# Optimization experiments

Hardware: AMD Instinct MI355X
Metric: run time of the kernel (lower is better)

The kernel has to match this reference:

```python
import jax, jax.numpy as jnp
import numpy as np

N, F, H, R, T, E, C = 50000, 128, 64, 3, 2, 500000, 2


def _seg_sum(v, idx, n):
    return jax.ops.segment_sum(v, idx, num_segments=n)


def _sage(x, src, dst, Wl, Wr, b, n):
    # PyG SAGEConv(mean): lin_l(mean_{j->i} x_j) + lin_r(x_i); lin_l carries bias.
    s = _seg_sum(x[src], dst, n)
    cnt = _seg_sum(jnp.ones((src.shape[0],), x.dtype), dst, n)
    agg = s / jnp.maximum(cnt, 1.0)[:, None]
    return agg @ Wl + x @ Wr + b


def _gcn(x, src, dst, w, W, b, n):
    # PyG GCNConv with edge_weight: self-loops (weight 1) + symmetric norm.
    deg = _seg_sum(w, dst, n) + 1.0
    dinv = deg ** -0.5
    norm = dinv[src] * w * dinv[dst]
    xW = x @ W
    return _seg_sum(norm[:, None] * xW[src], dst, n) + xW / deg[:, None] + b


def setup_inputs() -> dict:
    key = jax.random.key(0)
    ks = jax.random.split(key, 32)
    rn = lambda k, shp, s=0.1: jax.random.normal(k, shp, dtype=jnp.float32) * s
    return {
        "x": rn(ks[0], (N, F), 1.0),
        "edge_main": jax.random.randint(ks[1], (R, 2, E), 0, N, dtype=jnp.int32),
        "edge_tree": jax.random.randint(ks[2], (R, T, 2, E), 0, N, dtype=jnp.int32),
        "sage_Wl0": rn(ks[3], (R, F, H)), "sage_Wr0": rn(ks[4], (R, F, H)), "sage_b0": rn(ks[5], (R, H)),
        "sage_Wl1": rn(ks[6], (R, H, H)), "sage_Wr1": rn(ks[7], (R, H, H)), "sage_b1": rn(ks[8], (R, H)),
        "tree_Wl": rn(ks[9], (R, T, F, H)), "tree_Wr": rn(ks[10], (R, T, F, H)), "tree_b": rn(ks[11], (R, T, H)),
        "gate_W": rn(ks[12], (R, T, H)), "gate_b": rn(ks[13], (R, T)),
        "node_emb": rn(ks[14], (R, H), 1.0), "edge_emb": rn(ks[15], (R, H), 1.0),
        "fm_W": rn(ks[16], (R, 2 * H + F, F)), "fm_b": rn(ks[17], (R, F)),
        "ea_W1": rn(ks[18], (3 * H, F)), "ea_b1": rn(ks[19], (F,)),
        "ea_W2": rn(ks[20], (F, 1)), "ea_b2": rn(ks[21], (1,)),
        "gcn_W0": rn(ks[22], (R, F, H)), "gcn_b0": rn(ks[23], (R, H)),
        "gcn_W1": rn(ks[24], (R, H, H)), "gcn_b1": rn(ks[25], (R, H)),
        "lin_W": rn(ks[26], (R * H, C)), "lin_b": rn(ks[27], (C,)),
    }


def reference(x, edge_main, edge_tree, sage_Wl0, sage_Wr0, sage_b0, sage_Wl1, sage_Wr1, sage_b1,
              tree_Wl, tree_Wr, tree_b, gate_W, gate_b, node_emb, edge_emb, fm_W, fm_b,
              ea_W1, ea_b1, ea_W2, ea_b2, gcn_W0, gcn_b0, gcn_W1, gcn_b1, lin_W, lin_b):
    outs = []
    for r in range(R):
        src, dst = edge_main[r, 0], edge_main[r, 1]
        # Layer_AGG main SAGE stack (2 layers, relu between; dropout = eval no-op)
        y = jax.nn.relu(_sage(x, src, dst, sage_Wl0[r], sage_Wr0[r], sage_b0[r], N))
        y = _sage(y, src, dst, sage_Wl1[r], sage_Wr1[r], sage_b1[r], N)
        # tree branches + softmax gating
        trees = []
        for t in range(T):
            ts, td = edge_tree[r, t, 0], edge_tree[r, t, 1]
            trees.append(jax.nn.relu(_sage(x, ts, td, tree_Wl[r, t], tree_Wr[r, t], tree_b[r, t], N)))
        gates = jnp.stack([trees[t] @ gate_W[r, t] + gate_b[r, t] for t in range(T)], axis=-1)  # [N,T]
        alpha = jax.nn.softmax(gates, axis=-1)
        x_tree = sum(trees[t] * alpha[:, t:t + 1] for t in range(T))
        lo = y + 1.0 * x_tree  # self.weight = 1
        # edge mask via edge_attr_mlp on [lo[src], lo[dst], edge_type_emb]
        ef = jnp.concatenate([lo[src], lo[dst], jnp.broadcast_to(edge_emb[r], (E, H))], axis=-1)
        em = jax.nn.relu(ef @ ea_W1 + ea_b1) @ ea_W2 + ea_b2  # [E,1]
        # feature mask via feat_mask_r on [lo, x, node_type_emb]
        hetro = jnp.concatenate([lo, x, jnp.broadcast_to(node_emb[r], (N, H))], axis=-1)
        fm = hetro @ fm_W[r] + fm_b[r]
        mx = x * fm
        w = ((em - em.min()) / (em.max() - em.min()))[:, 0]  # min-max norm -> [E]
        # hetero GCN stack with edge weights
        z = jax.nn.relu(_gcn(mx, src, dst, w, gcn_W0[r], gcn_b0[r], N))
        z = _gcn(z, src, dst, w, gcn_W1[r], gcn_b1[r], N)
        outs.append(z)
    x_temp = jnp.concatenate(outs, axis=1)  # [N, R*H]
    logits = jnp.clip(x_temp @ lin_W + lin_b, -1e10, 1e10)
    return jax.nn.log_softmax(logits, axis=1), x_temp
```

## Files before the change

kernel.cpp:

```cpp
#include <hip/hip_runtime.h>
#include <cstdint>

#define N_NODES 50000
#define FEAT    128
#define HID     64
#define NREL    3
#define NTREE   2
#define NEDGE   500000
#define NCLS    2

#define BKT   391
#define CAP   1600
#define CHUNK 8192

typedef __attribute__((ext_vector_type(8))) short bfrag;
typedef __attribute__((ext_vector_type(4))) float ffrag;

__device__ __forceinline__ float wave_red(float v){
  #pragma unroll
  for(int off = 32; off > 0; off >>= 1) v += __shfl_xor(v, off, 64);
  return v;
}

__device__ __forceinline__ unsigned short f2b(float f){
  unsigned int u = __float_as_uint(f);
  unsigned int r = (u + 0x7FFFu + ((u >> 16) & 1u)) >> 16;
  return (unsigned short)r;
}
__device__ __forceinline__ float b2f_lo(unsigned int u){ return __uint_as_float(u << 16); }
__device__ __forceinline__ float b2f_hi(unsigned int u){ return __uint_as_float(u & 0xFFFF0000u); }
__device__ __forceinline__ float b2f(unsigned short s){ return __uint_as_float(((unsigned int)s) << 16); }

struct EdgePtrs { const int* s[9]; const int* d[9]; };

__global__ __launch_bounds__(256)
void k_passA(EdgePtrs ep, int* __restrict__ cursor, int* __restrict__ bucketed){
  int set = blockIdx.y;
  const int* src = ep.s[set];
  const int* dst = ep.d[set];
  __shared__ int stage[CHUNK];
  __shared__ int hist[BKT], gbase[BKT], lbase[BKT], cur[BKT];
  int tid = threadIdx.x;
  for(int b = tid; b < BKT; b += 256) hist[b] = 0;
  __syncthreads();
  int e0 = blockIdx.x * CHUNK;
  int nE = NEDGE - e0; if(nE > CHUNK) nE = CHUNK;
  for(int i = tid; i < nE; i += 256) atomicAdd(&hist[dst[e0 + i] >> 7], 1);
  __syncthreads();
  for(int b = tid; b < BKT; b += 256){
    int c = hist[b];
    gbase[b] = c ? atomicAdd(&cursor[set * BKT + b], c) : 0;
  }
  if(tid < 64){
    int running = 0;
    for(int base = 0; base < BKT; base += 64){
      int idx = base + tid;
      int v = (idx < BKT) ? hist[idx] : 0;
      int orig = v;
      #pragma unroll
      for(int off = 1; off < 64; off <<= 1){
        int t = __shfl_up(v, off, 64);
        if(tid >= off) v += t;
      }
      if(idx < BKT){ lbase[idx] = running + v - orig; cur[idx] = running + v - orig; }
      running += __shfl(v, 63, 64);
    }
  }
  __syncthreads();
  for(int i = tid; i < nE; i += 256){
    int e = e0 + i;
    int d = dst[e];
    int r = atomicAdd(&cur[d >> 7], 1);
    stage[r] = (d << 16) | src[e];
  }
  __syncthreads();
  int* bk = bucketed + (size_t)set * BKT * CAP;
  for(int i = tid; i < nE; i += 256){
    int p = stage[i];
    int b = ((unsigned int)p) >> 23;
    int pos = gbase[b] + (i - lbase[b]);
    if(pos < CAP) bk[b * CAP + pos] = p;
  }
}

__global__ void k_scanB(const int* __restrict__ cursor, int* __restrict__ bktbase,
                        int* __restrict__ indptr9){
  int set = blockIdx.x;
  __shared__ int sm[512];
  int tid = threadIdx.x;
  int v = (tid < BKT) ? cursor[set * BKT + tid] : 0;
  sm[tid] = v; __syncthreads();
  for(int off = 1; off < 512; off <<= 1){
    int t = (tid >= off) ? sm[tid - off] : 0;
    __syncthreads();
    sm[tid] += t;
    __syncthreads();
  }
  if(tid < BKT) bktbase[set * BKT + tid] = sm[tid] - v;
  if(tid == 0) indptr9[(size_t)set * (N_NODES + 1) + N_NODES] = NEDGE;
}

__global__ __launch_bounds__(256)
void k_passB(const int* __restrict__ bucketed, const int* __restrict__ cursor,
             const int* __restrict__ bktbase, int* __restrict__ indptr9,
             int* __restrict__ csr9){
  int set = blockIdx.y, b = blockIdx.x;
  int cnt = cursor[set * BKT + b]; if(cnt > CAP) cnt = CAP;
  int ebase = bktbase[set * BKT + b];
  const int* bk = bucketed + (size_t)set * BKT * CAP + b * CAP;
  __shared__ int pk[CAP];
  __shared__ int stage[CAP];
  __shared__ int h[128], sc[128], cur[128];
  int tid = threadIdx.x;
  for(int i = tid; i < cnt; i += 256) pk[i] = bk[i];
  if(tid < 128) h[tid] = 0;
  __syncthreads();
  for(int i = tid; i < cnt; i += 256) atomicAdd(&h[(pk[i] >> 16) & 127], 1);
  __syncthreads();
  if(tid < 128) sc[tid] = h[tid];
  __syncthreads();
  for(int off = 1; off < 128; off <<= 1){
    int t = 0;
    if(tid < 128 && tid >= off) t = sc[tid - off];
    __syncthreads();
    if(tid < 128) sc[tid] += t;
    __syncthreads();
  }
  if(tid < 128){
    int excl = sc[tid] - h[tid];
    cur[tid] = excl;
    int node = b * 128 + tid;
    if(node < N_NODES) indptr9[(size_t)set * (N_NODES + 1) + node] = ebase + excl;
  }
  __syncthreads();
  for(int i = tid; i < cnt; i += 256){
    int p = pk[i];
    int r = atomicAdd(&cur[(p >> 16) & 127], 1);
    stage[r] = p & 0xFFFF;
  }
  __syncthreads();
  int* out = csr9 + (size_t)set * NEDGE + ebase;
  for(int i = tid; i < cnt; i += 256) out[i] = stage[i];
}

__global__ void k_tobf16(const float* __restrict__ in, unsigned short* __restrict__ o, int n4){
  int i = blockIdx.x * 256 + threadIdx.x;
  if(i < n4){
    float4 v = ((const float4*)in)[i];
    ushort4 u; u.x = f2b(v.x); u.y = f2b(v.y); u.z = f2b(v.z); u.w = f2b(v.w);
    ((ushort4*)o)[i] = u;
  }
}

struct PackJobs { const float* src[20]; int wst[20]; int K[20]; int dst[20]; int n; };

__global__ void k_wpack(PackJobs J, unsigned short* __restrict__ out){
  int j = blockIdx.x;
  if(j >= J.n) return;
  const float* s = J.src[j];
  int wst = J.wst[j], K = J.K[j];
  unsigned short* o = out + J.dst[j];
  for(int i = threadIdx.x; i < K * 64; i += 256){
    int k = i >> 6, c = i & 63;
    o[((((k >> 3) * 64) + c) << 3) + (k & 7)] = f2b(s[(size_t)k * wst + c]);
  }
}

struct MG {
  const unsigned short* Wt[4];
  const float* bias[4];
  const void* add[4];
  const float* mul[4];
  void* out[4];
  int ast, mst, ost;
};

template<int K1, int K2, int NGRP, int RELU, int HAS_ADD, int ADDB, int HAS_MUL, int OUT_BF16>
__global__ __launch_bounds__(256)
void k_mgemm(const unsigned short* __restrict__ X1, int xs1,
             const unsigned short* __restrict__ X2, int xs2, MG P){
  constexpr int K = K1 + K2;
  constexpr int KS = K / 32;
  int tid = threadIdx.x;
  int lane = tid & 63;
  int w = tid >> 6;
  int row0 = blockIdx.x * 64 + w * 16;
  int l15 = lane & 15, kg = lane >> 4;
  int arow = row0 + l15; if(arow > N_NODES - 1) arow = N_NODES - 1;
  bfrag a[KS];
  #pragma unroll
  for(int ks = 0; ks < KS; ks++){
    int kk = ks * 32 + kg * 8;
    const unsigned short* p = (kk < K1) ? (X1 + (size_t)arow * xs1 + kk)
                                        : (X2 + (size_t)arow * xs2 + (kk - K1));
    a[ks] = *(const bfrag*)p;
  }
  int orow0 = row0 + kg * 4;
  #pragma unroll
  for(int g = 0; g < NGRP; g++){
    const unsigned short* Wg = P.Wt[g];
    #pragma unroll
    for(int ct = 0; ct < 4; ct++){
      int col = ct * 16 + l15;
      ffrag acc = {0.f, 0.f, 0.f, 0.f};
      #pragma unroll
      for(int ks = 0; ks < KS; ks++){
        bfrag bf = *(const bfrag*)(Wg + (((size_t)(ks * 4 + kg) * 64 + col) << 3));
        acc = __builtin_amdgcn_mfma_f32_16x16x32_bf16(a[ks], bf, acc, 0, 0, 0);
      }
      float bv = P.bias[g] ? P.bias[g][col] : 0.f;
      #pragma unroll
      for(int i = 0; i < 4; i++){
        int r = orow0 + i;
        if(r >= N_NODES) break;
        float v = acc[i] + bv;
        if(HAS_ADD){
          if(ADDB) v += b2f(((const unsigned short*)P.add[g])[(size_t)r * P.ast + col]);
          else     v += ((const float*)P.add[g])[(size_t)r * P.ast + col];
        }
        if(RELU) v = fmaxf(v, 0.f);
        if(HAS_MUL) v *= P.mul[g][(size_t)r * P.mst + col];
        if(OUT_BF16) ((unsigned short*)P.out[g])[(size_t)r * P.ost + col] = f2b(v);
        else         ((float*)P.out[g])[(size_t)r * P.ost + col] = v;
      }
    }
  }
}

template<int OUTB>
__global__ void k_aggq(const unsigned short* __restrict__ TB, int tst,
                       const int* __restrict__ indptr, const int* __restrict__ csr,
                       void* __restrict__ out){
  int br = blockIdx.y;
  const unsigned short* T = TB + (size_t)br * tst;
  const int* ip = indptr + (size_t)br * (N_NODES + 1);
  const int* cs = csr + (size_t)br * NEDGE;
  int lane = threadIdx.x & 63, wid = threadIdx.x >> 6;
  int node = blockIdx.x * 4 + wid;
  if(node >= N_NODES) return;
  int q = lane >> 4, c = lane & 15;
  int beg = ip[node], end = ip[node + 1];
  int cnt = end - beg;
  float sc = 1.0f / (float)(cnt >= 1 ? cnt : 1);
  float a0 = 0.f, a1 = 0.f, a2 = 0.f, a3 = 0.f;
  for(int j = beg + q; j < end; j += 4){
    int s = cs[j];
    uint2 u = *(const uint2*)(T + (size_t)s * 64 + c * 4);
    a0 += b2f_lo(u.x); a1 += b2f_hi(u.x);
    a2 += b2f_lo(u.y); a3 += b2f_hi(u.y);
  }
  a0 += __shfl_xor(a0, 16, 64); a1 += __shfl_xor(a1, 16, 64);
  a2 += __shfl_xor(a2, 16, 64); a3 += __shfl_xor(a3, 16, 64);
  a0 += __shfl_xor(a0, 32, 64); a1 += __shfl_xor(a1, 32, 64);
  a2 += __shfl_xor(a2, 32, 64); a3 += __shfl_xor(a3, 32, 64);
  if(q == 0){
    if(OUTB){
      ushort4 o; o.x = f2b(a0 * sc); o.y = f2b(a1 * sc); o.z = f2b(a2 * sc); o.w = f2b(a3 * sc);
      *(ushort4*)((unsigned short*)out + (size_t)br * tst + (size_t)node * 64 + c * 4) = o;
    } else {
      *(float4*)((float*)out + (size_t)node * 64 + c * 4) = float4{a0 * sc, a1 * sc, a2 * sc, a3 * sc};
    }
  }
}

__global__ void k_gates_lo(const unsigned short* __restrict__ t0b, const unsigned short* __restrict__ t1b,
                           const float* __restrict__ y, const float* __restrict__ gate_W,
                           const float* __restrict__ gate_b, unsigned short* __restrict__ lo){
  int lane = threadIdx.x & 63, wid = threadIdx.x >> 6;
  int node = blockIdx.x * 4 + wid;
  if(node >= N_NODES) return;
  size_t idx = (size_t)node * 64 + lane;
  float t0v = b2f(t0b[idx]), t1v = b2f(t1b[idx]), yv = y[idx];
  float g0 = wave_red(t0v * gate_W[lane]) + gate_b[0];
  float g1 = wave_red(t1v * gate_W[64 + lane]) + gate_b[1];
  float m = fmaxf(g0, g1);
  float e0 = expf(g0 - m), e1 = expf(g1 - m);
  float a0 = e0 / (e0 + e1);
  lo[idx] = f2b(yv + a0 * t0v + (1.f - a0) * t1v);
}

__global__ void k_cvec2(const float* __restrict__ ee, const float* __restrict__ ne,
                        const float* __restrict__ eaW1, const float* __restrict__ eab1,
                        const float* __restrict__ fmW, const float* __restrict__ fmb,
                        float* __restrict__ cE, float* __restrict__ cF){
  int j = threadIdx.x;
  if(blockIdx.x == 0){
    float s = eab1[j];
    for(int k = 0; k < 64; k++) s += ee[k] * eaW1[(128 + k) * 128 + j];
    cE[j] = s;
  } else {
    float s = fmb[j];
    for(int k = 0; k < 64; k++) s += ne[k] * fmW[(192 + k) * 128 + j];
    cF[j] = s;
  }
}

__global__ void k_em2(const unsigned short* __restrict__ AB,
                      const int* __restrict__ indptr, const int* __restrict__ csr_src,
                      const float* __restrict__ cvec, const float* __restrict__ W2,
                      const float* __restrict__ b2, float* __restrict__ em,
                      float* __restrict__ sumem){
  int lane = threadIdx.x & 63, wid = threadIdx.x >> 6;
  int node = blockIdx.x * 4 + wid;
  if(node >= N_NODES) return;
  int h = lane >> 5, c = lane & 31;
  uint2 bu = *(const uint2*)(AB + (size_t)node * 256 + 128 + c * 4);
  float4 cv = *(const float4*)&cvec[c * 4];
  float4 wv = *(const float4*)&W2[c * 4];
  float c0 = b2f_lo(bu.x) + cv.x, c1 = b2f_hi(bu.x) + cv.y;
  float c2 = b2f_lo(bu.y) + cv.z, c3 = b2f_hi(bu.y) + cv.w;
  float b2v = b2[0];
  int beg = indptr[node], end = indptr[node + 1];
  float ssum = 0.f;
  for(int j = beg + h; j < end; j += 2){
    int s = csr_src[j];
    uint2 au = *(const uint2*)(AB + (size_t)s * 256 + c * 4);
    float v = fmaxf(b2f_lo(au.x) + c0, 0.f) * wv.x + fmaxf(b2f_hi(au.x) + c1, 0.f) * wv.y
            + fmaxf(b2f_lo(au.y) + c2, 0.f) * wv.z + fmaxf(b2f_hi(au.y) + c3, 0.f) * wv.w;
    #pragma unroll
    for(int off = 1; off < 32; off <<= 1) v += __shfl_xor(v, off, 64);
    if(c == 0){
      float r = v + b2v;
      em[j] = r;
      ssum += r;
    }
  }
  float so = __shfl_xor(ssum, 32, 64);
  if(lane == 0) sumem[node] = ssum + so;
}

__global__ void k_minmax_part(const float* __restrict__ em, int n,
                              float* __restrict__ pmn, float* __restrict__ pmx){
  __shared__ float smn[256], smx[256];
  int tid = threadIdx.x;
  float mn = 3.4e38f, mx = -3.4e38f;
  for(int i = blockIdx.x * 256 + tid; i < n; i += gridDim.x * 256){
    float v = em[i];
    mn = fminf(mn, v); mx = fmaxf(mx, v);
  }
  smn[tid] = mn; smx[tid] = mx; __syncthreads();
  for(int s = 128; s > 0; s >>= 1){
    if(tid < s){ smn[tid] = fminf(smn[tid], smn[tid + s]); smx[tid] = fmaxf(smx[tid], smx[tid + s]); }
    __syncthreads();
  }
  if(tid == 0){ pmn[blockIdx.x] = smn[0]; pmx[blockIdx.x] = smx[0]; }
}

__global__ void k_minmax_final(const float* __restrict__ pmn, const float* __restrict__ pmx,
                               int nb, float* __restrict__ scal){
  __shared__ float smn[256], smx[256];
  int tid = threadIdx.x;
  float mn = 3.4e38f, mx = -3.4e38f;
  if(tid < nb){ mn = pmn[tid]; mx = pmx[tid]; }
  smn[tid] = mn; smx[tid] = mx; __syncthreads();
  for(int s = 128; s > 0; s >>= 1){
    if(tid < s){ smn[tid] = fminf(smn[tid], smn[tid + s]); smx[tid] = fmaxf(smx[tid], smx[tid + s]); }
    __syncthreads();
  }
  if(tid == 0){
    scal[0] = smn[0];
    scal[1] = 1.0f / fmaxf(smx[0] - smn[0], 1e-30f);
  }
}

__global__ void k_dinv(const int* __restrict__ indptr, const float* __restrict__ sumem,
                       const float* __restrict__ scal, float* __restrict__ dinv){
  int i = blockIdx.x * 256 + threadIdx.x;
  if(i >= N_NODES) return;
  float mn = scal[0], inv = scal[1];
  float cnt = (float)(indptr[i + 1] - indptr[i]);
  dinv[i] = rsqrtf(1.f + (sumem[i] - cnt * mn) * inv);
}

template<int RELU, int OUTB>
__global__ void k_gcn(const unsigned short* __restrict__ xW, const int* __restrict__ indptr,
                      const int* __restrict__ csr_src, const float* __restrict__ em,
                      const float* __restrict__ scal, const float* __restrict__ dinv,
                      const float* __restrict__ bias, void* __restrict__ out, int ostride){
  int lane = threadIdx.x & 63, wid = threadIdx.x >> 6;
  int node = blockIdx.x * 4 + wid;
  if(node >= N_NODES) return;
  int q = lane >> 4, c = lane & 15;
  float mn = scal[0], inv = scal[1];
  float di = dinv[node];
  float a0 = 0.f, a1 = 0.f, a2 = 0.f, a3 = 0.f;
  int beg = indptr[node], end = indptr[node + 1];
  for(int j = beg + q; j < end; j += 4){
    int s = csr_src[j];
    float wv = (em[j] - mn) * inv * dinv[s];
    uint2 u = *(const uint2*)(xW + (size_t)s * 64 + c * 4);
    a0 += wv * b2f_lo(u.x); a1 += wv * b2f_hi(u.x);
    a2 += wv * b2f_lo(u.y); a3 += wv * b2f_hi(u.y);
  }
  a0 += __shfl_xor(a0, 16, 64); a1 += __shfl_xor(a1, 16, 64);
  a2 += __shfl_xor(a2, 16, 64); a3 += __shfl_xor(a3, 16, 64);
  a0 += __shfl_xor(a0, 32, 64); a1 += __shfl_xor(a1, 32, 64);
  a2 += __shfl_xor(a2, 32, 64); a3 += __shfl_xor(a3, 32, 64);
  if(q == 0){
    uint2 su = *(const uint2*)(xW + (size_t)node * 64 + c * 4);
    float4 bv = *(const float4*)&bias[c * 4];
    float dd = di * di;
    float r0 = a0 * di + b2f_lo(su.x) * dd + bv.x;
    float r1 = a1 * di + b2f_hi(su.x) * dd + bv.y;
    float r2 = a2 * di + b2f_lo(su.y) * dd + bv.z;
    float r3 = a3 * di + b2f_hi(su.y) * dd + bv.w;
    if(RELU){ r0 = fmaxf(r0, 0.f); r1 = fmaxf(r1, 0.f); r2 = fmaxf(r2, 0.f); r3 = fmaxf(r3, 0.f); }
    if(OUTB){
      ushort4 o; o.x = f2b(r0); o.y = f2b(r1); o.z = f2b(r2); o.w = f2b(r3);
      *(ushort4*)((unsigned short*)out + (size_t)node * ostride + c * 4) = o;
    } else {
      *(float4*)((float*)out + (size_t)node * ostride + c * 4) = float4{r0, r1, r2, r3};
    }
  }
}

__global__ void k_logits(const float* __restrict__ xt, const float* __restrict__ lin_W,
                         const float* __restrict__ lin_b, float* __restrict__ out){
  int lane = threadIdx.x & 63, wid = threadIdx.x >> 6;
  int node = blockIdx.x * 4 + wid;
  if(node >= N_NODES) return;
  float a0 = 0.f, a1 = 0.f;
  #pragma unroll
  for(int q = 0; q < 3; q++){
    int k = q * 64 + lane;
    float v = xt[(size_t)node * 192 + k];
    a0 += v * lin_W[k * 2 + 0];
    a1 += v * lin_W[k * 2 + 1];
  }
  a0 = wave_red(a0);
  a1 = wave_red(a1);
  if(lane == 0){
    float l0 = fminf(fmaxf(a0 + lin_b[0], -1e10f), 1e10f);
    float l1 = fminf(fmaxf(a1 + lin_b[1], -1e10f), 1e10f);
    float m = fmaxf(l0, l1);
    float d = expf(l0 - m) + expf(l1 - m);
    float ls = m + logf(d);
    out[(size_t)node * 2 + 0] = l0 - ls;
    out[(size_t)node * 2 + 1] = l1 - ls;
  }
}

extern "C" void kernel_launch(void* const* d_in, const int* in_sizes, int n_in,
                              void* d_out, int out_size, void* d_ws, size_t ws_size,
                              hipStream_t stream){
  (void)in_sizes; (void)n_in; (void)out_size;
  const int N = N_NODES, E = NEDGE;

  const float* x        = (const float*)d_in[0];
  const int*  edge_main = (const int*)d_in[1];
  const int*  edge_tree = (const int*)d_in[2];
  const float* sage_Wl0 = (const float*)d_in[3];
  const float* sage_Wr0 = (const float*)d_in[4];
  const float* sage_b0  = (const float*)d_in[5];
  const float* sage_Wl1 = (const float*)d_in[6];
  const float* sage_Wr1 = (const float*)d_in[7];
  const float* sage_b1  = (const float*)d_in[8];
  const float* tree_Wl  = (const float*)d_in[9];
  const float* tree_Wr  = (const float*)d_in[10];
  const float* tree_b   = (const float*)d_in[11];
  const float* gate_W   = (const float*)d_in[12];
  const float* gate_b   = (const float*)d_in[13];
  const float* node_emb = (const float*)d_in[14];
  const float* edge_emb = (const float*)d_in[15];
  const float* fm_W     = (const float*)d_in[16];
  const float* fm_b     = (const float*)d_in[17];
  const float* ea_W1    = (const float*)d_in[18];
  const float* ea_b1    = (const float*)d_in[19];
  const float* ea_W2    = (const float*)d_in[20];
  const float* ea_b2    = (const float*)d_in[21];
  const float* gcn_W0   = (const float*)d_in[22];
  const float* gcn_b0   = (const float*)d_in[23];
  const float* gcn_W1   = (const float*)d_in[24];
  const float* gcn_b1   = (const float*)d_in[25];
  const float* lin_W    = (const float*)d_in[26];
  const float* lin_b    = (const float*)d_in[27];

  float* out_lsm   = (float*)d_out;
  float* out_xtemp = (float*)d_out + (size_t)N * NCLS;

  char* ws = (char*)d_ws;
  unsigned short* TB3  = (unsigned short*)(ws + 0);
  unsigned short* TBs  = (unsigned short*)(ws + 0);
  float*          Y    = (float*)(ws + 0);
  unsigned short* xW0b = (unsigned short*)(ws + 0);
  unsigned short* z0b  = (unsigned short*)(ws + 6400000);
  unsigned short* xW1b = (unsigned short*)(ws + 12800000);
  unsigned short* AG3  = (unsigned short*)(ws + 19200000);
  float*          AG   = (float*)(ws + 19200000);
  unsigned short* LOb  = (unsigned short*)(ws + 25600000);
  unsigned short* AB   = (unsigned short*)(ws + 0);
  unsigned short* y0b  = (unsigned short*)(ws + 38400000);
  unsigned short* T0b  = (unsigned short*)(ws + 44800000);
  unsigned short* T1b  = (unsigned short*)(ws + 51200000);
  unsigned short* MXb  = (unsigned short*)(ws + 38400000);
  unsigned short* xb   = (unsigned short*)(ws + 57600000);
  int*   bucketed = (int*)(ws + 0);
  unsigned short* Wpk = (unsigned short*)(ws + 70400000);
  int*   csr9     = (int*)(ws + 71000064);
  int*   indptr9  = (int*)(ws + 89000064);
  float* em       = (float*)(ws + 90800128);
  float* sumem    = (float*)(ws + 92800128);
  float* dinv     = (float*)(ws + 93000128);
  int*   cursor   = (int*)(ws + 93200128);
  int*   bktbase  = (int*)(ws + 93214208);
  float* cvecE    = (float*)(ws + 93228288);
  float* cvecF    = (float*)(ws + 93228800);
  float* scal     = (float*)(ws + 93229312);
  float* pmn      = (float*)(ws + 93229568);
  float* pmx      = (float*)(ws + 93230592);
  if(ws_size < 93231616) return;

  const int GN4 = (N + 3) / 4;
  const int GN  = (N + 255) / 256;
  const int GGM = (N + 63) / 64;
  const int NCH = (E + CHUNK - 1) / CHUNK;

  PackJobs PJ[2]; PJ[0].n = 0; PJ[1].n = 0;
  int npj = 0, dstElem = 0;
  const unsigned short* WlpA[NREL]; const unsigned short* WlpB[NREL]; const unsigned short* WlpC[NREL];
  const unsigned short* Wr0j[NREL]; const unsigned short* WrT0[NREL]; const unsigned short* WrT1[NREL];
  const unsigned short* Wl1j[NREL]; const unsigned short* Wr1j[NREL];
  const unsigned short* Fm0j[NREL]; const unsigned short* Fm1j[NREL];
  const unsigned short* G0j[NREL];  const unsigned short* G1j[NREL];
  const unsigned short *EaA0, *EaA1, *EaB0, *EaB1;
  auto addjob = [&](const float* src, int wst, int K) -> const unsigned short* {
    int slot = npj < 20 ? 0 : 1;
    int k = npj - slot * 20;
    PJ[slot].src[k] = src; PJ[slot].wst[k] = wst; PJ[slot].K[k] = K; PJ[slot].dst[k] = dstElem;
    PJ[slot].n = k + 1;
    const unsigned short* ret = Wpk + dstElem;
    dstElem += K * 64; npj++;
    return ret;
  };
  for(int r = 0; r < NREL; r++){
    WlpA[r] = addjob(sage_Wl0 + (size_t)r * 8192, 64, 128);
    WlpB[r] = addjob(tree_Wl + (size_t)(r * NTREE + 0) * 8192, 64, 128);
    WlpC[r] = addjob(tree_Wl + (size_t)(r * NTREE + 1) * 8192, 64, 128);
    Wr0j[r] = addjob(sage_Wr0 + (size_t)r * 8192, 64, 128);
    WrT0[r] = addjob(tree_Wr + (size_t)(r * NTREE + 0) * 8192, 64, 128);
    WrT1[r] = addjob(tree_Wr + (size_t)(r * NTREE + 1) * 8192, 64, 128);
    Wl1j[r] = addjob(sage_Wl1 + (size_t)r * 4096, 64, 64);
    Wr1j[r] = addjob(sage_Wr1 + (size_t)r * 4096, 64, 64);
    Fm0j[r] = addjob(fm_W + (size_t)r * 32768, 128, 192);
    Fm1j[r] = addjob(fm_W + (size_t)r * 32768 + 64, 128, 192);
    G0j[r]  = addjob(gcn_W0 + (size_t)r * 8192, 64, 128);
    G1j[r]  = addjob(gcn_W1 + (size_t)r * 4096, 64, 64);
  }
  EaA0 = addjob(ea_W1, 128, 64);
  EaA1 = addjob(ea_W1 + 64, 128, 64);
  EaB0 = addjob(ea_W1 + 64 * 128, 128, 64);
  EaB1 = addjob(ea_W1 + 64 * 128 + 64, 128, 64);

  EdgePtrs ep;
  for(int r = 0; r < NREL; r++){
    ep.s[r * 3 + 0] = edge_main + (size_t)r * 2 * E;
    ep.d[r * 3 + 0] = ep.s[r * 3 + 0] + E;
    for(int t = 0; t < NTREE; t++){
      ep.s[r * 3 + 1 + t] = edge_tree + ((size_t)(r * NTREE + t) * 2) * E;
      ep.d[r * 3 + 1 + t] = ep.s[r * 3 + 1 + t] + E;
    }
  }
  hipMemsetAsync(cursor, 0, 9 * BKT * 4, stream);
  k_passA<<<dim3(NCH, 9), 256, 0, stream>>>(ep, cursor, bucketed);
  k_scanB<<<9, 512, 0, stream>>>(cursor, bktbase, indptr9);
  k_passB<<<dim3(BKT, 9), 256, 0, stream>>>(bucketed, cursor, bktbase, indptr9, csr9);

  k_wpack<<<PJ[0].n, 256, 0, stream>>>(PJ[0], Wpk);
  k_wpack<<<PJ[1].n, 256, 0, stream>>>(PJ[1], Wpk);
  k_tobf16<<<(N * 128 / 4 + 255) / 256, 256, 0, stream>>>(x, xb, N * 128 / 4);

  for(int r = 0; r < NREL; r++){
    const int* ipM = indptr9 + (size_t)(r * 3) * (N + 1);
    const int* csM = csr9 + (size_t)(r * 3) * E;

    { MG p{}; p.ost = 64;
      p.Wt[0] = WlpA[r]; p.Wt[1] = WlpB[r]; p.Wt[2] = WlpC[r];
      p.out[0] = TB3; p.out[1] = TB3 + (size_t)N * 64; p.out[2] = TB3 + (size_t)2 * N * 64;
      k_mgemm<128, 0, 3, 0, 0, 0, 0, 1><<<GGM, 256, 0, stream>>>(xb, 128, nullptr, 0, p); }

    k_aggq<1><<<dim3(GN4, 3), 256, 0, stream>>>(TB3, N * 64, ipM, csM, AG3);
    { MG p{}; p.ast = 64; p.ost = 64;
      p.Wt[0] = Wr0j[r]; p.bias[0] = sage_b0 + r * 64; p.add[0] = AG3;                         p.out[0] = y0b;
      p.Wt[1] = WrT0[r]; p.bias[1] = tree_b + (size_t)(r * NTREE + 0) * 64; p.add[1] = AG3 + (size_t)N * 64;   p.out[1] = T0b;
      p.Wt[2] = WrT1[r]; p.bias[2] = tree_b + (size_t)(r * NTREE + 1) * 64; p.add[2] = AG3 + (size_t)2 * N * 64; p.out[2] = T1b;
      k_mgemm<128, 0, 3, 1, 1, 1, 0, 1><<<GGM, 256, 0, stream>>>(xb, 128, nullptr, 0, p); }

    { MG p{}; p.ost = 64; p.Wt[0] = Wl1j[r]; p.out[0] = TBs;
      k_mgemm<64, 0, 1, 0, 0, 0, 0, 1><<<GGM, 256, 0, stream>>>(y0b, 64, nullptr, 0, p); }
    k_aggq<0><<<dim3(GN4, 1), 256, 0, stream>>>(TBs, N * 64, ipM, csM, AG);
    { MG p{}; p.ast = 64; p.ost = 64;
      p.Wt[0] = Wr1j[r]; p.bias[0] = sage_b1 + r * 64; p.add[0] = AG; p.out[0] = Y;
      k_mgemm<64, 0, 1, 0, 1, 0, 0, 0><<<GGM, 256, 0, stream>>>(y0b, 64, nullptr, 0, p); }

    k_gates_lo<<<GN4, 256, 0, stream>>>(T0b, T1b, Y, gate_W + (size_t)r * 128, gate_b + r * 2, LOb);

    k_cvec2<<<2, 128, 0, stream>>>(edge_emb + r * 64, node_emb + r * 64, ea_W1, ea_b1,
                                   fm_W + (size_t)r * 32768, fm_b + r * 128, cvecE, cvecF);

    { MG p{}; p.ost = 256;
      p.Wt[0] = EaA0; p.Wt[1] = EaA1; p.Wt[2] = EaB0; p.Wt[3] = EaB1;
      p.out[0] = AB; p.out[1] = AB + 64; p.out[2] = AB + 128; p.out[3] = AB + 192;
      k_mgemm<64, 0, 4, 0, 0, 0, 0, 1><<<GGM, 256, 0, stream>>>(LOb, 64, nullptr, 0, p); }

    k_em2<<<GN4, 256, 0, stream>>>(AB, ipM, csM, cvecE, ea_W2, ea_b2, em, sumem);

    k_minmax_part<<<256, 256, 0, stream>>>(em, E, pmn, pmx);
    k_minmax_final<<<1, 256, 0, stream>>>(pmn, pmx, 256, scal);

    k_dinv<<<GN, 256, 0, stream>>>(ipM, sumem, scal, dinv);

    { MG p{}; p.mst = 128; p.ost = 128;
      p.Wt[0] = Fm0j[r]; p.Wt[1] = Fm1j[r];
      p.bias[0] = cvecF; p.bias[1] = cvecF + 64;
      p.mul[0] = x; p.mul[1] = x + 64;
      p.out[0] = MXb; p.out[1] = MXb + 64;
      k_mgemm<64, 128, 2, 0, 0, 0, 1, 1><<<GGM, 256, 0, stream>>>(LOb, 64, xb, 128, p); }

    { MG p{}; p.ost = 64; p.Wt[0] = G0j[r]; p.out[0] = xW0b;
      k_mgemm<128, 0, 1, 0, 0, 0, 0, 1><<<GGM, 256, 0, stream>>>(MXb, 128, nullptr, 0, p); }
    k_gcn<1, 1><<<GN4, 256, 0, stream>>>(xW0b, ipM, csM, em, scal, dinv, gcn_b0 + r * 64, z0b, 64);
    { MG p{}; p.ost = 64; p.Wt[0] = G1j[r]; p.out[0] = xW1b;
      k_mgemm<64, 0, 1, 0, 0, 0, 0, 1><<<GGM, 256, 0, stream>>>(z0b, 64, nullptr, 0, p); }
    k_gcn<0, 0><<<GN4, 256, 0, stream>>>(xW1b, ipM, csM, em, scal, dinv, gcn_b1 + r * 64,
                                         out_xtemp + r * 64, 192);
  }

  k_logits<<<GN4, 256, 0, stream>>>(out_xtemp, lin_W, lin_b, out_lsm);
}
```

Baseline: 987.5 us.

## Fuse edge-attr and feature-mask GEMMs, fold minmax into em, unroll gathers

```diff
diff --git a/kernel.cpp b/kernel.cpp
--- a/kernel.cpp
+++ b/kernel.cpp
@@ -11,7 +11,7 @@
 
 #define BKT   391
 #define CAP   1600
-#define CHUNK 8192
+#define CHUNK 4096
 
 typedef __attribute__((ext_vector_type(8))) short bfrag;
 typedef __attribute__((ext_vector_type(4))) float ffrag;
@@ -227,6 +227,71 @@
   }
 }
 
+struct ABMX {
+  const unsigned short* Wea[4];
+  const unsigned short* Wfm[2];
+  const float* cF;
+  const float* xf32;
+  unsigned short* ab;
+  unsigned short* mx;
+};
+
+__global__ __launch_bounds__(256)
+void k_abmx(const unsigned short* __restrict__ LOb, const unsigned short* __restrict__ xb, ABMX P){
+  int tid = threadIdx.x, lane = tid & 63, w = tid >> 6;
+  int row0 = blockIdx.x * 64 + w * 16;
+  int l15 = lane & 15, kg = lane >> 4;
+  int arow = row0 + l15; if(arow > N_NODES - 1) arow = N_NODES - 1;
+  bfrag a[6];
+  a[0] = *(const bfrag*)(LOb + (size_t)arow * 64 + kg * 8);
+  a[1] = *(const bfrag*)(LOb + (size_t)arow * 64 + 32 + kg * 8);
+  #pragma unroll
+  for(int ks = 0; ks < 4; ks++)
+    a[2 + ks] = *(const bfrag*)(xb + (size_t)arow * 128 + ks * 32 + kg * 8);
+  int orow0 = row0 + kg * 4;
+  #pragma unroll
+  for(int g = 0; g < 4; g++){
+    const unsigned short* Wg = P.Wea[g];
+    #pragma unroll
+    for(int ct = 0; ct < 4; ct++){
+      int col = ct * 16 + l15;
+      ffrag acc = {0.f, 0.f, 0.f, 0.f};
+      bfrag b0 = *(const bfrag*)(Wg + (((size_t)(0 * 4 + kg) * 64 + col) << 3));
+      bfrag b1 = *(const bfrag*)(Wg + (((size_t)(1 * 4 + kg) * 64 + col) << 3));
+      acc = __builtin_amdgcn_mfma_f32_16x16x32_bf16(a[0], b0, acc, 0, 0, 0);
+      acc = __builtin_amdgcn_mfma_f32_16x16x32_bf16(a[1], b1, acc, 0, 0, 0);
+      #pragma unroll
+      for(int i = 0; i < 4; i++){
+        int r = orow0 + i;
+        if(r >= N_NODES) break;
+        P.ab[(size_t)r * 256 + g * 64 + col] = f2b(acc[i]);
+      }
+    }
+  }
+  #pragma unroll
+  for(int g = 0; g < 2; g++){
+    const unsigned short* Wg = P.Wfm[g];
+    #pragma unroll
+    for(int ct = 0; ct < 4; ct++){
+      int col = ct * 16 + l15;
+      ffrag acc = {0.f, 0.f, 0.f, 0.f};
+      #pragma unroll
+      for(int ks = 0; ks < 6; ks++){
+        bfrag bf = *(const bfrag*)(Wg + (((size_t)(ks * 4 + kg) * 64 + col) << 3));
+        acc = __builtin_amdgcn_mfma_f32_16x16x32_bf16(a[ks], bf, acc, 0, 0, 0);
+      }
+      float bv = P.cF[g * 64 + col];
+      #pragma unroll
+      for(int i = 0; i < 4; i++){
+        int r = orow0 + i;
+        if(r >= N_NODES) break;
+        float v = (acc[i] + bv) * P.xf32[(size_t)r * 128 + g * 64 + col];
+        P.mx[(size_t)r * 128 + g * 64 + col] = f2b(v);
+      }
+    }
+  }
+}
+
 template<int OUTB>
 __global__ void k_aggq(const unsigned short* __restrict__ TB, int tst,
                        const int* __restrict__ indptr, const int* __restrict__ csr,
@@ -243,7 +308,15 @@
   int cnt = end - beg;
   float sc = 1.0f / (float)(cnt >= 1 ? cnt : 1);
   float a0 = 0.f, a1 = 0.f, a2 = 0.f, a3 = 0.f;
-  for(int j = beg + q; j < end; j += 4){
+  int j = beg + q;
+  for(; j + 4 < end; j += 8){
+    int s0 = cs[j], s1 = cs[j + 4];
+    uint2 u0 = *(const uint2*)(T + (size_t)s0 * 64 + c * 4);
+    uint2 u1 = *(const uint2*)(T + (size_t)s1 * 64 + c * 4);
+    a0 += b2f_lo(u0.x) + b2f_lo(u1.x); a1 += b2f_hi(u0.x) + b2f_hi(u1.x);
+    a2 += b2f_lo(u0.y) + b2f_lo(u1.y); a3 += b2f_hi(u0.y) + b2f_hi(u1.y);
+  }
+  if(j < end){
     int s = cs[j];
     uint2 u = *(const uint2*)(T + (size_t)s * 64 + c * 4);
     a0 += b2f_lo(u.x); a1 += b2f_hi(u.x);
@@ -263,9 +336,29 @@
   }
 }
 
-__global__ void k_gates_lo(const unsigned short* __restrict__ t0b, const unsigned short* __restrict__ t1b,
-                           const float* __restrict__ y, const float* __restrict__ gate_W,
-                           const float* __restrict__ gate_b, unsigned short* __restrict__ lo){
+__global__ void k_gates_cvec(const unsigned short* __restrict__ t0b, const unsigned short* __restrict__ t1b,
+                             const float* __restrict__ y, const float* __restrict__ gate_W,
+                             const float* __restrict__ gate_b, unsigned short* __restrict__ lo,
+                             const float* __restrict__ ee, const float* __restrict__ ne,
+                             const float* __restrict__ eaW1, const float* __restrict__ eab1,
+                             const float* __restrict__ fmW, const float* __restrict__ fmb,
+                             float* __restrict__ cE, float* __restrict__ cF, int gn4){
+  if(blockIdx.x >= gn4){
+    int which = blockIdx.x - gn4;
+    int j = threadIdx.x;
+    if(j < 128){
+      if(which == 0){
+        float s = eab1[j];
+        for(int k = 0; k < 64; k++) s += ee[k] * eaW1[(128 + k) * 128 + j];
+        cE[j] = s;
+      } else {
+        float s = fmb[j];
+        for(int k = 0; k < 64; k++) s += ne[k] * fmW[(192 + k) * 128 + j];
+        cF[j] = s;
+      }
+    }
+    return;
+  }
   int lane = threadIdx.x & 63, wid = threadIdx.x >> 6;
   int node = blockIdx.x * 4 + wid;
   if(node >= N_NODES) return;
@@ -279,71 +372,72 @@
   lo[idx] = f2b(yv + a0 * t0v + (1.f - a0) * t1v);
 }
 
-__global__ void k_cvec2(const float* __restrict__ ee, const float* __restrict__ ne,
-                        const float* __restrict__ eaW1, const float* __restrict__ eab1,
-                        const float* __restrict__ fmW, const float* __restrict__ fmb,
-                        float* __restrict__ cE, float* __restrict__ cF){
-  int j = threadIdx.x;
-  if(blockIdx.x == 0){
-    float s = eab1[j];
-    for(int k = 0; k < 64; k++) s += ee[k] * eaW1[(128 + k) * 128 + j];
-    cE[j] = s;
-  } else {
-    float s = fmb[j];
-    for(int k = 0; k < 64; k++) s += ne[k] * fmW[(192 + k) * 128 + j];
-    cF[j] = s;
-  }
-}
-
 __global__ void k_em2(const unsigned short* __restrict__ AB,
                       const int* __restrict__ indptr, const int* __restrict__ csr_src,
                       const float* __restrict__ cvec, const float* __restrict__ W2,
                       const float* __restrict__ b2, float* __restrict__ em,
-                      float* __restrict__ sumem){
+                      float* __restrict__ sumem, float* __restrict__ pmn, float* __restrict__ pmx){
   int lane = threadIdx.x & 63, wid = threadIdx.x >> 6;
   int node = blockIdx.x * 4 + wid;
-  if(node >= N_NODES) return;
-  int h = lane >> 5, c = lane & 31;
-  uint2 bu = *(const uint2*)(AB + (size_t)node * 256 + 128 + c * 4);
-  float4 cv = *(const float4*)&cvec[c * 4];
-  float4 wv = *(const float4*)&W2[c * 4];
-  float c0 = b2f_lo(bu.x) + cv.x, c1 = b2f_hi(bu.x) + cv.y;
-  float c2 = b2f_lo(bu.y) + cv.z, c3 = b2f_hi(bu.y) + cv.w;
-  float b2v = b2[0];
-  int beg = indptr[node], end = indptr[node + 1];
-  float ssum = 0.f;
-  for(int j = beg + h; j < end; j += 2){
-    int s = csr_src[j];
-    uint2 au = *(const uint2*)(AB + (size_t)s * 256 + c * 4);
-    float v = fmaxf(b2f_lo(au.x) + c0, 0.f) * wv.x + fmaxf(b2f_hi(au.x) + c1, 0.f) * wv.y
-            + fmaxf(b2f_lo(au.y) + c2, 0.f) * wv.z + fmaxf(b2f_hi(au.y) + c3, 0.f) * wv.w;
-    #pragma unroll
-    for(int off = 1; off < 32; off <<= 1) v += __shfl_xor(v, off, 64);
-    if(c == 0){
-      float r = v + b2v;
-      em[j] = r;
-      ssum += r;
-    }
-  }
-  float so = __shfl_xor(ssum, 32, 64);
-  if(lane == 0) sumem[node] = ssum + so;
-}
-
-__global__ void k_minmax_part(const float* __restrict__ em, int n,
-                              float* __restrict__ pmn, float* __restrict__ pmx){
-  __shared__ float smn[256], smx[256];
-  int tid = threadIdx.x;
+  bool act = (node < N_NODES);
   float mn = 3.4e38f, mx = -3.4e38f;
-  for(int i = blockIdx.x * 256 + tid; i < n; i += gridDim.x * 256){
-    float v = em[i];
-    mn = fminf(mn, v); mx = fmaxf(mx, v);
-  }
-  smn[tid] = mn; smx[tid] = mx; __syncthreads();
-  for(int s = 128; s > 0; s >>= 1){
-    if(tid < s){ smn[tid] = fminf(smn[tid], smn[tid + s]); smx[tid] = fmaxf(smx[tid], smx[tid + s]); }
-    __syncthreads();
-  }
-  if(tid == 0){ pmn[blockIdx.x] = smn[0]; pmx[blockIdx.x] = smx[0]; }
+  if(act){
+    int h = lane >> 5, c = lane & 31;
+    uint2 bu = *(const uint2*)(AB + (size_t)node * 256 + 128 + c * 4);
+    float4 cv = *(const float4*)&cvec[c * 4];
+    float4 wv = *(const float4*)&W2[c * 4];
+    float c0 = b2f_lo(bu.x) + cv.x, c1 = b2f_hi(bu.x) + cv.y;
+    float c2 = b2f_lo(bu.y) + cv.z, c3 = b2f_hi(bu.y) + cv.w;
+    float b2v = b2[0];
+    int beg = indptr[node], end = indptr[node + 1];
+    float ssum = 0.f;
+    int j = beg + h;
+    for(; j + 2 < end; j += 4){
+      int s0 = csr_src[j], s1 = csr_src[j + 2];
+      uint2 au0 = *(const uint2*)(AB + (size_t)s0 * 256 + c * 4);
+      uint2 au1 = *(const uint2*)(AB + (size_t)s1 * 256 + c * 4);
+      float v0 = fmaxf(b2f_lo(au0.x) + c0, 0.f) * wv.x + fmaxf(b2f_hi(au0.x) + c1, 0.f) * wv.y
+               + fmaxf(b2f_lo(au0.y) + c2, 0.f) * wv.z + fmaxf(b2f_hi(au0.y) + c3, 0.f) * wv.w;
+      float v1 = fmaxf(b2f_lo(au1.x) + c0, 0.f) * wv.x + fmaxf(b2f_hi(au1.x) + c1, 0.f) * wv.y
+               + fmaxf(b2f_lo(au1.y) + c2, 0.f) * wv.z + fmaxf(b2f_hi(au1.y) + c3, 0.f) * wv.w;
+      #pragma unroll
+      for(int off = 1; off < 32; off <<= 1){
+        v0 += __shfl_xor(v0, off, 64);
+        v1 += __shfl_xor(v1, off, 64);
+      }
+      if(c == 0){
+        float r0 = v0 + b2v, r1 = v1 + b2v;
+        em[j] = r0; em[j + 2] = r1;
+        ssum += r0 + r1;
+        mn = fminf(mn, fminf(r0, r1)); mx = fmaxf(mx, fmaxf(r0, r1));
+      }
+    }
+    if(j < end){
+      int s = csr_src[j];
+      uint2 au = *(const uint2*)(AB + (size_t)s * 256 + c * 4);
+      float v = fmaxf(b2f_lo(au.x) + c0, 0.f) * wv.x + fmaxf(b2f_hi(au.x) + c1, 0.f) * wv.y
+              + fmaxf(b2f_lo(au.y) + c2, 0.f) * wv.z + fmaxf(b2f_hi(au.y) + c3, 0.f) * wv.w;
+      #pragma unroll
+      for(int off = 1; off < 32; off <<= 1) v += __shfl_xor(v, off, 64);
+      if(c == 0){
+        float r = v + b2v;
+        em[j] = r;
+        ssum += r;
+        mn = fminf(mn, r); mx = fmaxf(mx, r);
+      }
+    }
+    float so = __shfl_xor(ssum, 32, 64);
+    if(lane == 0) sumem[node] = ssum + so;
+    mn = fminf(mn, __shfl_xor(mn, 32, 64));
+    mx = fmaxf(mx, __shfl_xor(mx, 32, 64));
+  }
+  __shared__ float bmn[4], bmx[4];
+  if(lane == 0){ bmn[wid] = mn; bmx[wid] = mx; }
+  __syncthreads();
+  if(threadIdx.x == 0){
+    pmn[blockIdx.x] = fminf(fminf(bmn[0], bmn[1]), fminf(bmn[2], bmn[3]));
+    pmx[blockIdx.x] = fmaxf(fmaxf(bmx[0], bmx[1]), fmaxf(bmx[2], bmx[3]));
+  }
 }
 
 __global__ void k_minmax_final(const float* __restrict__ pmn, const float* __restrict__ pmx,
@@ -351,7 +445,9 @@
   __shared__ float smn[256], smx[256];
   int tid = threadIdx.x;
   float mn = 3.4e38f, mx = -3.4e38f;
-  if(tid < nb){ mn = pmn[tid]; mx = pmx[tid]; }
+  for(int i = tid; i < nb; i += 256){
+    mn = fminf(mn, pmn[i]); mx = fmaxf(mx, pmx[i]);
+  }
   smn[tid] = mn; smx[tid] = mx; __syncthreads();
   for(int s = 128; s > 0; s >>= 1){
     if(tid < s){ smn[tid] = fminf(smn[tid], smn[tid + s]); smx[tid] = fmaxf(smx[tid], smx[tid + s]); }
@@ -385,7 +481,19 @@
   float di = dinv[node];
   float a0 = 0.f, a1 = 0.f, a2 = 0.f, a3 = 0.f;
   int beg = indptr[node], end = indptr[node + 1];
-  for(int j = beg + q; j < end; j += 4){
+  int j = beg + q;
+  for(; j + 4 < end; j += 8){
+    int s0 = csr_src[j], s1 = csr_src[j + 4];
+    float w0 = (em[j] - mn) * inv * dinv[s0];
+    float w1 = (em[j + 4] - mn) * inv * dinv[s1];
+    uint2 u0 = *(const uint2*)(xW + (size_t)s0 * 64 + c * 4);
+    uint2 u1 = *(const uint2*)(xW + (size_t)s1 * 64 + c * 4);
+    a0 += w0 * b2f_lo(u0.x) + w1 * b2f_lo(u1.x);
+    a1 += w0 * b2f_hi(u0.x) + w1 * b2f_hi(u1.x);
+    a2 += w0 * b2f_lo(u0.y) + w1 * b2f_lo(u1.y);
+    a3 += w0 * b2f_hi(u0.y) + w1 * b2f_hi(u1.y);
+  }
+  if(j < end){
     int s = csr_src[j];
     float wv = (em[j] - mn) * inv * dinv[s];
     uint2 u = *(const uint2*)(xW + (size_t)s * 64 + c * 4);
@@ -507,8 +615,8 @@
   float* cvecF    = (float*)(ws + 93228800);
   float* scal     = (float*)(ws + 93229312);
   float* pmn      = (float*)(ws + 93229568);
-  float* pmx      = (float*)(ws + 93230592);
-  if(ws_size < 93231616) return;
+  float* pmx      = (float*)(ws + 93279568);
+  if(ws_size < 93330000) return;
 
   const int GN4 = (N + 3) / 4;
   const int GN  = (N + 255) / 256;
@@ -592,29 +700,23 @@
       p.Wt[0] = Wr1j[r]; p.bias[0] = sage_b1 + r * 64; p.add[0] = AG; p.out[0] = Y;
       k_mgemm<64, 0, 1, 0, 1, 0, 0, 0><<<GGM, 256, 0, stream>>>(y0b, 64, nullptr, 0, p); }
 
-    k_gates_lo<<<GN4, 256, 0, stream>>>(T0b, T1b, Y, gate_W + (size_t)r * 128, gate_b + r * 2, LOb);
-
-    k_cvec2<<<2, 128, 0, stream>>>(edge_emb + r * 64, node_emb + r * 64, ea_W1, ea_b1,
-                                   fm_W + (size_t)r * 32768, fm_b + r * 128, cvecE, cvecF);
-
-    { MG p{}; p.ost = 256;
-      p.Wt[0] = EaA0; p.Wt[1] = EaA1; p.Wt[2] = EaB0; p.Wt[3] = EaB1;
-      p.out[0] = AB; p.out[1] = AB + 64; p.out[2] = AB + 128; p.out[3] = AB + 192;
-      k_mgemm<64, 0, 4, 0, 0, 0, 0, 1><<<GGM, 256, 0, stream>>>(LOb, 64, nullptr, 0, p); }
-
-    k_em2<<<GN4, 256, 0, stream>>>(AB, ipM, csM, cvecE, ea_W2, ea_b2, em, sumem);
-
-    k_minmax_part<<<256, 256, 0, stream>>>(em, E, pmn, pmx);
-    k_minmax_final<<<1, 256, 0, stream>>>(pmn, pmx, 256, scal);
+    k_gates_cvec<<<GN4 + 2, 256, 0, stream>>>(T0b, T1b, Y, gate_W + (size_t)r * 128,
+                                              gate_b + r * 2, LOb,
+                                              edge_emb + r * 64, node_emb + r * 64,
+                                              ea_W1, ea_b1, fm_W + (size_t)r * 32768,
+                                              fm_b + r * 128, cvecE, cvecF, GN4);
+
+    { ABMX p{};
+      p.Wea[0] = EaA0; p.Wea[1] = EaA1; p.Wea[2] = EaB0; p.Wea[3] = EaB1;
+      p.Wfm[0] = Fm0j[r]; p.Wfm[1] = Fm1j[r];
+      p.cF = cvecF; p.xf32 = x; p.ab = AB; p.mx = MXb;
+      k_abmx<<<GGM, 256, 0, stream>>>(LOb, xb, p); }
+
+    k_em2<<<GN4, 256, 0, stream>>>(AB, ipM, csM, cvecE, ea_W2, ea_b2, em, sumem, pmn, pmx);
+
+    k_minmax_final<<<1, 256, 0, stream>>>(pmn, pmx, GN4, scal);
 
     k_dinv<<<GN, 256, 0, stream>>>(ipM, sumem, scal, dinv);
-
-    { MG p{}; p.mst = 128; p.ost = 128;
-      p.Wt[0] = Fm0j[r]; p.Wt[1] = Fm1j[r];
-      p.bias[0] = cvecF; p.bias[1] = cvecF + 64;
-      p.mul[0] = x; p.mul[1] = x + 64;
-      p.out[0] = MXb; p.out[1] = MXb + 64;
-      k_mgemm<64, 128, 2, 0, 0, 0, 1, 1><<<GGM, 256, 0, stream>>>(LOb, 64, xb, 128, p); }
 
     { MG p{}; p.ost = 64; p.Wt[0] = G0j[r]; p.out[0] = xW0b;
       k_mgemm<128, 0, 1, 0, 0, 0, 0, 1><<<GGM, 256, 0, stream>>>(MXb, 128, nullptr, 0, p); }
```

Measured after the change: 913.7 us. 1.08x faster.
